# Optimization experiments

Measured on AMD Instinct MI355X. Metric: run time of the kernel, lower is better.

The kernel has to match this reference:

```python
import jax, jax.numpy as jnp
import numpy as np

B, L, T = 32, 512, 400
EMB, PRE, ENC, ARNN, DRNN, NSYM = 512, 256, 512, 1024, 1024, 256
MEAN_COEFF, SCALE_COEFF = 1.0, 10.0


def setup_inputs() -> dict:
    key = jax.random.key(0)
    ks = jax.random.split(key, 20)
    s = 0.02
    inp = {
        'memory': jax.random.normal(ks[0], (B, L, ENC), jnp.float32),
        'decoder_inputs': jax.random.normal(ks[1], (B, EMB, T), jnp.float32),
        'memory_lengths': jax.random.randint(ks[2], (B,), L // 2, L + 1).astype(jnp.int64),
        # prenet
        'pW1': jax.random.normal(ks[3], (PRE, EMB), jnp.float32) * s,
        'pb1': jnp.zeros((PRE,), jnp.float32),
        'pW2': jax.random.normal(ks[4], (PRE, PRE), jnp.float32) * s,
        'pb2': jnp.zeros((PRE,), jnp.float32),
        # attention LSTMCell
        'aWih': jax.random.normal(ks[5], (4 * ARNN, PRE + ENC), jnp.float32) * s,
        'aWhh': jax.random.normal(ks[6], (4 * ARNN, ARNN), jnp.float32) * s,
        'abih': jnp.zeros((4 * ARNN,), jnp.float32),
        'abhh': jnp.zeros((4 * ARNN,), jnp.float32),
        # Gaussian attention param linear (weight zero-init in torch; small here)
        'attWp': jax.random.normal(ks[7], (2, ARNN), jnp.float32) * 0.001,
        'attbp': jnp.zeros((2,), jnp.float32),
        # decoder LSTMCell
        'dWih': jax.random.normal(ks[8], (4 * DRNN, ARNN + ENC), jnp.float32) * s,
        'dWhh': jax.random.normal(ks[9], (4 * DRNN, DRNN), jnp.float32) * s,
        'dbih': jnp.zeros((4 * DRNN,), jnp.float32),
        'dbhh': jnp.zeros((4 * DRNN,), jnp.float32),
        # output linear
        'oW': jax.random.normal(ks[10], (NSYM, DRNN + ENC), jnp.float32) * s,
        'ob': jnp.zeros((NSYM,), jnp.float32),
    }
    return inp


def _lstm_cell(x, h, c, Wih, Whh, bih, bhh):
    g = x @ Wih.T + bih + h @ Whh.T + bhh
    i, f, gg, o = jnp.split(g, 4, axis=-1)
    c = jax.nn.sigmoid(f) * c + jax.nn.sigmoid(i) * jnp.tanh(gg)
    h = jax.nn.sigmoid(o) * jnp.tanh(c)
    return h, c


def _decoder_core(memory, decoder_inputs, memory_lengths,
                  pW1, pb1, pW2, pb2,
                  aWih, aWhh, abih, abhh,
                  attWp, attbp,
                  dWih, dWhh, dbih, dbhh,
                  oW, ob):
    b = memory.shape[0]
    Lm = memory.shape[1]
    # go frame + time-major inputs -> prenet (dropout is identity in eval)
    x = jnp.transpose(decoder_inputs, (2, 0, 1))            # [T, B, EMB]
    x = jnp.concatenate([jnp.zeros((1, b, EMB), x.dtype), x], axis=0)  # [T+1, B, EMB]
    x = jax.nn.relu(x @ pW1.T + pb1)
    x = jax.nn.relu(x @ pW2.T + pb2)                        # [T+1, B, PRE]
    x = x[:T]                                               # loop runs T steps

    lin = jnp.arange(Lm, dtype=memory.dtype)[None, :]       # [1, L]
    pad_mask = lin >= memory_lengths[:, None].astype(memory.dtype)  # [B, L] True at pad

    def step(carry, x_t):
        ah, ac, dh, dc, ctx, mean = carry
        cell_in = jnp.concatenate([x_t, ctx], axis=1)
        ah, ac = _lstm_cell(cell_in, ah, ac, aWih, aWhh, abih, abhh)
        params = ah @ attWp.T + attbp                       # [B, 2]
        mean = mean + jnp.exp(params[:, 0:1]) * MEAN_COEFF  # [B, 1]
        scale = jnp.exp(params[:, 1:2]) * SCALE_COEFF       # [B, 1]
        Z = jnp.sqrt(2.0 * np.pi * scale ** 2)
        w = jnp.exp(-0.5 * (lin - mean) ** 2 / scale ** 2) / Z  # [B, L]
        w = jnp.where(pad_mask, 0.0, w)
        ctx = jnp.einsum('bl,bld->bd', w, memory)           # [B, ENC]
        dec_in = jnp.concatenate([ah, ctx], axis=1)
        dh, dc = _lstm_cell(dec_in, dh, dc, dWih, dWhh, dbih, dbhh)
        out = jnp.concatenate([dh, ctx], axis=1) @ oW.T + ob  # [B, NSYM]
        return (ah, ac, dh, dc, ctx, mean), (out, w, params)

    z = jnp.zeros
    carry0 = (z((b, ARNN)), z((b, ARNN)), z((b, DRNN)), z((b, DRNN)),
              z((b, ENC)), z((b, 1)))
    _, (logits, aligns, ps) = jax.lax.scan(step, carry0, x)
    # time-major -> [B, T, ...]
    return (jnp.transpose(logits, (1, 0, 2)),
            jnp.transpose(aligns, (1, 0, 2)),
            jnp.transpose(ps, (1, 0, 2)))


def reference(memory, decoder_inputs, memory_lengths,
              pW1, pb1, pW2, pb2,
              aWih, aWhh, abih, abhh,
              attWp, attbp,
              dWih, dWhh, dbih, dbhh,
              oW, ob):
    return _decoder_core(memory, decoder_inputs, memory_lengths,
                         pW1, pb1, pW2, pb2,
                         aWih, aWhh, abih, abhh,
                         attWp, attbp,
                         dWih, dWhh, dbih, dbhh,
                         oW, ob)
```

## Files before the change

### kernel.cpp

```cpp
#include <hip/hip_runtime.h>
#include <math.h>

#define Bsz   32
#define Lmem  512
#define Tsteps 400
#define EMBD  512
#define PRE   256
#define ENCD  512
#define ARNN  1024
#define DRNN  1024
#define NSYM  256

typedef _Float16 f16x8 __attribute__((ext_vector_type(8)));
typedef float    f32x4 __attribute__((ext_vector_type(4)));
typedef _Float16 half_t;

#define KA  (PRE + ENCD + ARNN)
#define KAQ (KA / 4)
#define NMA (KAQ / 32)
#define KD  (ARNN + ENCD + DRNN)
#define KDQ (KD / 4)
#define NMD (KDQ / 32)
#define LDA_A 1800
#define LDA_D 2568

__device__ __forceinline__ void st_agent_f16(half_t* p, half_t v) {
    __hip_atomic_store((unsigned short*)p, __builtin_bit_cast(unsigned short, v),
                       __ATOMIC_RELAXED, __HIP_MEMORY_SCOPE_AGENT);
}
__device__ __forceinline__ void st_agent_f32(float* p, float v) {
    __hip_atomic_store(p, v, __ATOMIC_RELAXED, __HIP_MEMORY_SCOPE_AGENT);
}
__device__ __forceinline__ void st_agent_u32(unsigned* p, unsigned v) {
    __hip_atomic_store(p, v, __ATOMIC_RELAXED, __HIP_MEMORY_SCOPE_AGENT);
}
__device__ __forceinline__ float ld_agent_f32(const float* p) {
    return __hip_atomic_load(p, __ATOMIC_RELAXED, __HIP_MEMORY_SCOPE_AGENT);
}
__device__ __forceinline__ unsigned ld_agent_u32(const unsigned* p) {
    return __hip_atomic_load(p, __ATOMIC_RELAXED, __HIP_MEMORY_SCOPE_AGENT);
}
__device__ __forceinline__ f16x8 ld_agent_f16x8(const half_t* p) {
    union { unsigned long long u[2]; f16x8 v; } c;
    c.u[0] = __hip_atomic_load((const unsigned long long*)p,
                               __ATOMIC_RELAXED, __HIP_MEMORY_SCOPE_AGENT);
    c.u[1] = __hip_atomic_load(((const unsigned long long*)p) + 1,
                               __ATOMIC_RELAXED, __HIP_MEMORY_SCOPE_AGENT);
    return c.v;
}

template<int KIH, int KHH>
__global__ __launch_bounds__(256) void conv_lstm_w(
    const float* __restrict__ Wih, const float* __restrict__ Whh,
    const float* __restrict__ bih, const float* __restrict__ bhh,
    half_t* __restrict__ Wcat, float* __restrict__ bsum)
{
    constexpr int K = KIH + KHH;
    const int j = blockIdx.x;
    const float* srcA = Wih + (size_t)j * KIH;
    const float* srcB = Whh + (size_t)j * KHH;
    half_t* dst = Wcat + (size_t)j * K;
    for (int k = threadIdx.x; k < KIH; k += 256) dst[k]       = (half_t)srcA[k];
    for (int k = threadIdx.x; k < KHH; k += 256) dst[KIH + k] = (half_t)srcB[k];
    if (threadIdx.x == 0) bsum[j] = bih[j] + bhh[j];
}

__global__ __launch_bounds__(256) void conv_mat(
    const float* __restrict__ src, half_t* __restrict__ dst, int n)
{
    for (int i = blockIdx.x * 256 + threadIdx.x; i < n; i += gridDim.x * 256)
        dst[i] = (half_t)src[i];
}

__global__ __launch_bounds__(256) void prenet_kernel(
    const float* __restrict__ din,
    const float* __restrict__ pW1, const float* __restrict__ pb1,
    const float* __restrict__ pW2, const float* __restrict__ pb2,
    half_t* __restrict__ xpre)
{
    __shared__ float xs[8][EMBD];
    __shared__ float h1s[8][PRE];
    const int tid = threadIdx.x;
    const int row0 = blockIdx.x * 8;

    for (int idx = tid; idx < 8 * EMBD; idx += 256) {
        int r = idx >> 9;
        int e = idx & 511;
        int rid = row0 + r;
        int t = rid >> 5;
        int b = rid & 31;
        float v = 0.f;
        if (t > 0) v = din[(size_t)b * EMBD * Tsteps + (size_t)e * Tsteps + (t - 1)];
        xs[r][e] = v;
    }
    __syncthreads();

    {
        float acc[8] = {0.f,0.f,0.f,0.f,0.f,0.f,0.f,0.f};
        const float* wr = pW1 + (size_t)tid * EMBD;
        for (int e = 0; e < EMBD; e += 4) {
            float4 wv = *(const float4*)(wr + e);
            #pragma unroll
            for (int r = 0; r < 8; ++r) {
                float4 xv = *(const float4*)&xs[r][e];
                acc[r] += wv.x * xv.x + wv.y * xv.y + wv.z * xv.z + wv.w * xv.w;
            }
        }
        float bias = pb1[tid];
        #pragma unroll
        for (int r = 0; r < 8; ++r) h1s[r][tid] = fmaxf(acc[r] + bias, 0.f);
    }
    __syncthreads();

    {
        float acc[8] = {0.f,0.f,0.f,0.f,0.f,0.f,0.f,0.f};
        const float* wr = pW2 + (size_t)tid * PRE;
        for (int e = 0; e < PRE; e += 4) {
            float4 wv = *(const float4*)(wr + e);
            #pragma unroll
            for (int r = 0; r < 8; ++r) {
                float4 xv = *(const float4*)&h1s[r][e];
                acc[r] += wv.x * xv.x + wv.y * xv.y + wv.z * xv.z + wv.w * xv.w;
            }
        }
        float bias = pb2[tid];
        #pragma unroll
        for (int r = 0; r < 8; ++r) {
            int rid = row0 + r;
            int t = rid >> 5;
            int b = rid & 31;
            xpre[(size_t)t * Bsz * PRE + (size_t)b * PRE + tid] =
                (half_t)fmaxf(acc[r] + bias, 0.f);
        }
    }
}

__device__ __forceinline__ void g_arrive(unsigned* flags, unsigned ph)
{
    asm volatile("s_waitcnt vmcnt(0)" ::: "memory");
    __syncthreads();
    if (threadIdx.x == 0)
        __hip_atomic_store(flags + blockIdx.x * 16, ph,
                           __ATOMIC_RELAXED, __HIP_MEMORY_SCOPE_AGENT);
}
__device__ __forceinline__ void g_wait(unsigned* flags, unsigned ph)
{
    if (threadIdx.x < 64) {
        const unsigned* f = flags + threadIdx.x * 64;
        for (;;) {
            unsigned a = ld_agent_u32(f);
            unsigned b = ld_agent_u32(f + 16);
            unsigned c = ld_agent_u32(f + 32);
            unsigned d = ld_agent_u32(f + 48);
            if (min(min(a, b), min(c, d)) >= ph) break;
            __builtin_amdgcn_s_sleep(2);
        }
    }
    __syncthreads();
}

__global__ __launch_bounds__(512, 1) void decoder_persistent(
    const half_t* __restrict__ Wcat_a, const float* __restrict__ bsum_a,
    const half_t* __restrict__ Wcat_d, const float* __restrict__ bsum_d,
    const half_t* __restrict__ Wo, const float* __restrict__ ob,
    const half_t* __restrict__ xpre,
    const float* __restrict__ attWp, const float* __restrict__ attbp,
    const int* __restrict__ mlen, const half_t* __restrict__ mem16,
    half_t* __restrict__ ah0, half_t* __restrict__ ah1,
    half_t* __restrict__ dh0, half_t* __restrict__ dh1,
    half_t* __restrict__ ctx0, half_t* __restrict__ ctx1,
    float* __restrict__ mean0, float* __restrict__ mean1,
    float* __restrict__ logits, float* __restrict__ aligns,
    float* __restrict__ ps,
    unsigned* flags)
{
    const int blk   = blockIdx.x;
    const int tid   = threadIdx.x;
    const int wave  = tid >> 6;
    const int lane  = tid & 63;
    const int btile = wave & 1;
    const int kq    = wave >> 1;
    const int m15   = lane & 15;
    const int kh    = lane >> 4;
    const int u0    = blk << 2;
    const int bb    = (btile << 4) + m15;

    __shared__ __align__(16) half_t wAl[16 * LDA_A];
    __shared__ __align__(16) half_t wDl[16 * LDA_D];
    __shared__ float gredA[4][2][16][16];
    __shared__ float gredD[4][2][16][16];
    __shared__ float wsh[Lmem];
    __shared__ float lred[16][33];
    __shared__ float wred8[8][2];
    __shared__ float bc2[2];

    for (int g = tid; g < 16 * (KA / 8); g += 512) {
        int r = g / (KA / 8);
        int c = (g - r * (KA / 8)) * 8;
        int jr = (r >> 2) * 1024 + u0 + (r & 3);
        *(f16x8*)(wAl + r * LDA_A + c) = *(const f16x8*)(Wcat_a + (size_t)jr * KA + c);
    }
    for (int g = tid; g < 16 * (KD / 8); g += 512) {
        int r = g / (KD / 8);
        int c = (g - r * (KD / 8)) * 8;
        int jr = (r >> 2) * 1024 + u0 + (r & 3);
        *(f16x8*)(wDl + r * LDA_D + c) = *(const f16x8*)(Wcat_d + (size_t)jr * KD + c);
    }
    float bsA[4] = {0.f,0.f,0.f,0.f}, bsD[4] = {0.f,0.f,0.f,0.f};
    float cA = 0.f, cD = 0.f;
    if (tid < 128) {
        const int ul = tid >> 5;
        #pragma unroll
        for (int gi = 0; gi < 4; ++gi) bsA[gi] = bsum_a[gi * 1024 + u0 + ul];
    } else if (tid < 256) {
        const int ul = (tid - 128) >> 5;
        #pragma unroll
        for (int gi = 0; gi < 4; ++gi) bsD[gi] = bsum_d[gi * 1024 + u0 + ul];
    }
    const half_t* lA = wAl + m15 * LDA_A + kq * KAQ + (kh << 3);
    const half_t* lD = wDl + m15 * LDA_D + kq * KDQ + (kh << 3);
    __syncthreads();

    f16x8 bvA[NMA], bvD[NMD];
    {
        const half_t* s0 = xpre;
        #pragma unroll
        for (int i = 0; i < NMA; ++i) {
            const int kg = kq * KAQ + i * 32 + (kh << 3);
            if (kg < PRE)             bvA[i] = *(const f16x8*)(s0 + bb * PRE + kg);
            else if (kg < PRE + ENCD) bvA[i] = ld_agent_f16x8(ctx1 + bb * ENCD + (kg - PRE));
            else                      bvA[i] = ld_agent_f16x8(ah1 + bb * ARNN + (kg - PRE - ENCD));
        }
    }

    unsigned ph = 0;

    for (int t = 0; t <= Tsteps; ++t) {
        const int par = t & 1;
        half_t*       ah_cur  = par ? ah1 : ah0;
        half_t*       ctx_cur = par ? ctx1 : ctx0;
        const half_t* ctx_prv = par ? ctx0 : ctx1;
        float*        mn_cur  = par ? mean1 : mean0;
        const float*  mn_prv  = par ? mean0 : mean1;
        half_t*       dh_s    = par ? dh0 : dh1;

        if (t < Tsteps) {
            f32x4 accA = {0.f,0.f,0.f,0.f};
            #pragma unroll
            for (int i = 0; i < NMA; ++i) {
                f16x8 av = *(const f16x8*)(lA + i * 32);
                accA = __builtin_amdgcn_mfma_f32_16x16x32_f16(av, bvA[i], accA, 0, 0, 0);
            }
            #pragma unroll
            for (int r = 0; r < 4; ++r)
                gredA[kq][btile][(kh << 2) + r][m15] = accA[r];
        }
        if (t > 0) {
            f32x4 accD = {0.f,0.f,0.f,0.f};
            #pragma unroll
            for (int i = 0; i < NMD; ++i) {
                f16x8 av = *(const f16x8*)(lD + i * 32);
                accD = __builtin_amdgcn_mfma_f32_16x16x32_f16(av, bvD[i], accD, 0, 0, 0);
            }
            #pragma unroll
            for (int r = 0; r < 4; ++r)
                gredD[kq][btile][(kh << 2) + r][m15] = accD[r];
        }
        __syncthreads();
        if (tid < 128) {
            if (t < Tsteps) {
                const int ul = tid >> 5;
                const int bq = tid & 31;
                const int bt = bq >> 4;
                const int nn = bq & 15;
                float g[4];
                #pragma unroll
                for (int gi = 0; gi < 4; ++gi) {
                    const int mr = (gi << 2) + ul;
                    g[gi] = gredA[0][bt][mr][nn] + gredA[1][bt][mr][nn]
                          + gredA[2][bt][mr][nn] + gredA[3][bt][mr][nn] + bsA[gi];
                }
                float si = 1.f / (1.f + expf(-g[0]));
                float sf = 1.f / (1.f + expf(-g[1]));
                float so = 1.f / (1.f + expf(-g[3]));
                cA = sf * cA + si * tanhf(g[2]);
                st_agent_f16(&ah_cur[bq * 1024 + u0 + ul], (half_t)(so * tanhf(cA)));
            }
        } else if (tid < 256) {
            if (t > 0) {
                const int lt = tid - 128;
                const int ul = lt >> 5;
                const int bq = lt & 31;
                const int bt = bq >> 4;
                const int nn = bq & 15;
                float g[4];
                #pragma unroll
                for (int gi = 0; gi < 4; ++gi) {
                    const int mr = (gi << 2) + ul;
                    g[gi] = gredD[0][bt][mr][nn] + gredD[1][bt][mr][nn]
                          + gredD[2][bt][mr][nn] + gredD[3][bt][mr][nn] + bsD[gi];
                }
                float si = 1.f / (1.f + expf(-g[0]));
                float sf = 1.f / (1.f + expf(-g[1]));
                float so = 1.f / (1.f + expf(-g[3]));
                cD = sf * cD + si * tanhf(g[2]);
                st_agent_f16(&dh_s[bq * 1024 + u0 + ul], (half_t)(so * tanhf(cD)));
            }
        }
        ++ph; g_arrive(flags, ph); g_wait(flags, ph);

        if (t < Tsteps) {
            const int abt = blk >> 3;
            const int dt  = blk & 7;
            float p0, p1;
            {
                union { unsigned u; _Float16 h[2]; } a;
                a.u = ld_agent_u32((const unsigned*)(ah_cur + abt * ARNN + 2 * tid));
                float a0 = (float)a.h[0], a1 = (float)a.h[1];
                float2 w0 = *(const float2*)(attWp + 2 * tid);
                float2 w1 = *(const float2*)(attWp + ARNN + 2 * tid);
                p0 = a0 * w0.x + a1 * w0.y;
                p1 = a0 * w1.x + a1 * w1.y;
            }
            #pragma unroll
            for (int off = 32; off > 0; off >>= 1) {
                p0 += __shfl_down(p0, off, 64);
                p1 += __shfl_down(p1, off, 64);
            }
            if (lane == 0) { wred8[wave][0] = p0; wred8[wave][1] = p1; }
            __syncthreads();
            if (tid == 0) {
                float q0 = attbp[0], q1 = attbp[1];
                #pragma unroll
                for (int w = 0; w < 8; ++w) { q0 += wred8[w][0]; q1 += wred8[w][1]; }
                float mn = ld_agent_f32(&mn_prv[abt]) + expf(q0) * 1.0f;
                float sc = expf(q1) * 10.0f;
                if (dt == 0) {
                    st_agent_f32(&mn_cur[abt], mn);
                    st_agent_f32(&ps[(size_t)abt * Tsteps * 2 + (size_t)t * 2 + 0], q0);
                    st_agent_f32(&ps[(size_t)abt * Tsteps * 2 + (size_t)t * 2 + 1], q1);
                }
                bc2[0] = mn; bc2[1] = sc;
            }
            __syncthreads();
            const float mn = bc2[0], sc = bc2[1];
            const float inv_s = 1.f / sc;
            const float coef = 0.3989422804014327f * inv_s;
            const int len = mlen[abt];
            {
                float z = ((float)tid - mn) * inv_s;
                float wv = (tid < len) ? expf(-0.5f * z * z) * coef : 0.f;
                wsh[tid] = wv;
                if (dt == 0)
                    st_agent_f32(&aligns[(size_t)abt * Tsteps * Lmem + (size_t)t * Lmem + tid], wv);
            }
            __syncthreads();
            int lo = (int)fmaxf(0.f, floorf(mn - 9.f * sc));
            int hi = (int)fminf((float)len, ceilf(mn + 9.f * sc) + 1.f);
            const int d8 = (dt << 6) + (wave << 3);
            const half_t* mb = mem16 + (size_t)abt * Lmem * ENCD + d8;
            float acc[8] = {0.f,0.f,0.f,0.f,0.f,0.f,0.f,0.f};
            for (int l = lo + lane; l < hi; l += 64) {
                f16x8 mv = *(const f16x8*)(mb + (size_t)l * ENCD);
                float w = wsh[l];
                #pragma unroll
                for (int j = 0; j < 8; ++j) acc[j] += w * (float)mv[j];
            }
            #pragma unroll
            for (int off = 32; off > 0; off >>= 1) {
                #pragma unroll
                for (int j = 0; j < 8; ++j) acc[j] += __shfl_down(acc[j], off, 64);
            }
            if (lane == 0) {
                #pragma unroll
                for (int j = 0; j < 4; ++j) {
                    union { unsigned u; _Float16 h[2]; } pk;
                    pk.h[0] = (_Float16)acc[2 * j];
                    pk.h[1] = (_Float16)acc[2 * j + 1];
                    st_agent_u32((unsigned*)(ctx_cur + abt * ENCD + d8 + 2 * j), pk.u);
                }
            }
        }
        if (t > 0) {
            const int b_o = tid & 31;
            const int ks  = tid >> 5;
            const half_t* wrow = Wo + (size_t)blk * (DRNN + ENCD) + ks * 96;
            float outacc = 0.f;
            #pragma unroll
            for (int half = 0; half < 2; ++half) {
                f16x8 wv[6], av[6];
                #pragma unroll
                for (int c8 = 0; c8 < 6; ++c8) {
                    const int cc = half * 6 + c8;
                    const int k = ks * 96 + cc * 8;
                    wv[c8] = *(const f16x8*)(wrow + cc * 8);
                    const half_t* ap = (k < DRNN) ? (dh_s + b_o * DRNN + k)
                                                  : (ctx_prv + b_o * ENCD + (k - DRNN));
                    av[c8] = ld_agent_f16x8(ap);
                }
                #pragma unroll
                for (int c8 = 0; c8 < 6; ++c8)
                    #pragma unroll
                    for (int e = 0; e < 8; ++e)
                        outacc += (float)wv[c8][e] * (float)av[c8][e];
            }
            lred[ks][b_o] = outacc;
            __syncthreads();
            if (tid < 32) {
                float s = 0.f;
                #pragma unroll
                for (int q = 0; q < 16; ++q) s += lred[q][tid];
                st_agent_f32(&logits[(size_t)tid * Tsteps * NSYM + (size_t)(t - 1) * NSYM + blk],
                             s + ob[blk]);
            }
        }
        if (t < Tsteps) {
            ++ph; g_arrive(flags, ph);
            if (t + 1 < Tsteps) {
                const half_t* s0n = xpre + (size_t)(t + 1) * Bsz * PRE;
                #pragma unroll
                for (int i = 0; i < NMA; ++i) {
                    const int kg = kq * KAQ + i * 32 + (kh << 3);
                    if (kg < PRE)
                        bvA[i] = *(const f16x8*)(s0n + bb * PRE + kg);
                    else if (kg >= PRE + ENCD)
                        bvA[i] = ld_agent_f16x8(ah_cur + bb * ARNN + (kg - PRE - ENCD));
                }
            }
            #pragma unroll
            for (int i = 0; i < NMD; ++i) {
                const int kg = kq * KDQ + i * 32 + (kh << 3);
                if (kg < ARNN)
                    bvD[i] = ld_agent_f16x8(ah_cur + bb * ARNN + kg);
                else if (kg >= ARNN + ENCD)
                    bvD[i] = ld_agent_f16x8(dh_s + bb * DRNN + (kg - ARNN - ENCD));
            }
            g_wait(flags, ph);
            if (t + 1 < Tsteps) {
                #pragma unroll
                for (int i = 0; i < NMA; ++i) {
                    const int kg = kq * KAQ + i * 32 + (kh << 3);
                    if (kg >= PRE && kg < PRE + ENCD)
                        bvA[i] = ld_agent_f16x8(ctx_cur + bb * ENCD + (kg - PRE));
                }
            }
            #pragma unroll
            for (int i = 0; i < NMD; ++i) {
                const int kg = kq * KDQ + i * 32 + (kh << 3);
                if (kg >= ARNN && kg < ARNN + ENCD)
                    bvD[i] = ld_agent_f16x8(ctx_cur + bb * ENCD + (kg - ARNN));
            }
        }
    }
}

extern "C" void kernel_launch(void* const* d_in, const int* in_sizes, int n_in,
                              void* d_out, int out_size, void* d_ws, size_t ws_size,
                              hipStream_t stream)
{
    (void)in_sizes; (void)n_in; (void)out_size; (void)ws_size;
    const float* memory = (const float*)d_in[0];
    const float* din    = (const float*)d_in[1];
    const int*   mlen   = (const int*)d_in[2];
    const float* pW1    = (const float*)d_in[3];
    const float* pb1    = (const float*)d_in[4];
    const float* pW2    = (const float*)d_in[5];
    const float* pb2    = (const float*)d_in[6];
    const float* aWih   = (const float*)d_in[7];
    const float* aWhh   = (const float*)d_in[8];
    const float* abih   = (const float*)d_in[9];
    const float* abhh   = (const float*)d_in[10];
    const float* attWp  = (const float*)d_in[11];
    const float* attbp  = (const float*)d_in[12];
    const float* dWih   = (const float*)d_in[13];
    const float* dWhh   = (const float*)d_in[14];
    const float* dbih   = (const float*)d_in[15];
    const float* dbhh   = (const float*)d_in[16];
    const float* oW     = (const float*)d_in[17];
    const float* ob     = (const float*)d_in[18];

    float* logits = (float*)d_out;
    float* aligns = logits + (size_t)Bsz * Tsteps * NSYM;
    float* ps     = aligns + (size_t)Bsz * Tsteps * Lmem;

    char* base = (char*)d_ws;
    auto alloc = [&](size_t bytes) -> char* {
        char* p = base; base += (bytes + 255) & ~(size_t)255; return p;
    };
    half_t* Wcat_a = (half_t*)alloc((size_t)4096 * KA * 2);
    half_t* Wcat_d = (half_t*)alloc((size_t)4096 * KD * 2);
    half_t* Wo     = (half_t*)alloc((size_t)NSYM * (DRNN + ENCD) * 2);
    float*  bsum_a = (float*)alloc(4096 * 4);
    float*  bsum_d = (float*)alloc(4096 * 4);
    half_t* xpre   = (half_t*)alloc((size_t)Tsteps * Bsz * PRE * 2);
    half_t* mem16  = (half_t*)alloc((size_t)Bsz * Lmem * ENCD * 2);
    half_t* ah0    = (half_t*)alloc(Bsz * ARNN * 2);
    half_t* ah1    = (half_t*)alloc(Bsz * ARNN * 2);
    half_t* dh0    = (half_t*)alloc(Bsz * DRNN * 2);
    half_t* dh1    = (half_t*)alloc(Bsz * DRNN * 2);
    half_t* ctx0   = (half_t*)alloc(Bsz * ENCD * 2);
    half_t* ctx1   = (half_t*)alloc(Bsz * ENCD * 2);
    float*  mean0  = (float*)alloc(Bsz * 4);
    float*  mean1  = (float*)alloc(Bsz * 4);
    unsigned* flags = (unsigned*)alloc(256 * 16 * 4);

    (void)hipMemsetAsync(ah1,   0, Bsz * ARNN * 2, stream);
    (void)hipMemsetAsync(dh1,   0, Bsz * DRNN * 2, stream);
    (void)hipMemsetAsync(ctx1,  0, Bsz * ENCD * 2, stream);
    (void)hipMemsetAsync(mean0, 0, Bsz * 4, stream);
    (void)hipMemsetAsync(mean1, 0, Bsz * 4, stream);
    (void)hipMemsetAsync(flags, 0, 256 * 16 * 4, stream);

    conv_lstm_w<PRE + ENCD, ARNN><<<4096, 256, 0, stream>>>(
        aWih, aWhh, abih, abhh, Wcat_a, bsum_a);
    conv_lstm_w<ARNN + ENCD, DRNN><<<4096, 256, 0, stream>>>(
        dWih, dWhh, dbih, dbhh, Wcat_d, bsum_d);
    conv_mat<<<768, 256, 0, stream>>>(oW, Wo, NSYM * (DRNN + ENCD));
    conv_mat<<<4096, 256, 0, stream>>>(memory, mem16, Bsz * Lmem * ENCD);
    prenet_kernel<<<Tsteps * Bsz / 8, 256, 0, stream>>>(din, pW1, pb1, pW2, pb2, xpre);

    decoder_persistent<<<256, 512, 0, stream>>>(
        Wcat_a, bsum_a, Wcat_d, bsum_d, Wo, ob, xpre,
        attWp, attbp, mlen, mem16,
        ah0, ah1, dh0, dh1, ctx0, ctx1, mean0, mean1,
        logits, aligns, ps,
        flags);
}
```

Measured before the change: 14.29 ms.

## Replace flat grid barrier with two-level tree barrier and pin prefetched operands

The grid barrier used to have every one of the 256 blocks poll all 256 arrival flags. It is now a hierarchy: 16 aggregator blocks each watch 16 flags, block 0 watches the 16 aggregates, and everyone else polls a single release flag. This cuts polling traffic on the flags in the per-step barrier, but adds two extra serial hops of latency. An empty asm constraint is also added on the prefetched operand vectors so their loads are issued before the barrier and not sunk past it.

```diff
diff --git a/kernel.cpp b/kernel.cpp
--- a/kernel.cpp
+++ b/kernel.cpp
@@ -48,6 +48,7 @@
                                __ATOMIC_RELAXED, __HIP_MEMORY_SCOPE_AGENT);
     return c.v;
 }
+__device__ __forceinline__ void keep16(f16x8& v) { asm volatile("" : "+v"(v)); }
 
 template<int KIH, int KHH>
 __global__ __launch_bounds__(256) void conv_lstm_w(
@@ -140,21 +141,25 @@
     asm volatile("s_waitcnt vmcnt(0)" ::: "memory");
     __syncthreads();
     if (threadIdx.x == 0)
-        __hip_atomic_store(flags + blockIdx.x * 16, ph,
-                           __ATOMIC_RELAXED, __HIP_MEMORY_SCOPE_AGENT);
+        st_agent_u32(flags + blockIdx.x * 16, ph);
 }
 __device__ __forceinline__ void g_wait(unsigned* flags, unsigned ph)
 {
-    if (threadIdx.x < 64) {
-        const unsigned* f = flags + threadIdx.x * 64;
-        for (;;) {
-            unsigned a = ld_agent_u32(f);
-            unsigned b = ld_agent_u32(f + 16);
-            unsigned c = ld_agent_u32(f + 32);
-            unsigned d = ld_agent_u32(f + 48);
-            if (min(min(a, b), min(c, d)) >= ph) break;
-            __builtin_amdgcn_s_sleep(2);
-        }
+    if (blockIdx.x < 16 && threadIdx.x < 16) {
+        const unsigned* f = flags + (blockIdx.x * 16 + threadIdx.x) * 16;
+        while (ld_agent_u32(f) < ph) __builtin_amdgcn_s_sleep(1);
+        if (threadIdx.x == 0)
+            st_agent_u32(flags + (256 + blockIdx.x) * 16, ph);
+    }
+    if (blockIdx.x == 0 && threadIdx.x < 16) {
+        const unsigned* f2 = flags + (256 + threadIdx.x) * 16;
+        while (ld_agent_u32(f2) < ph) __builtin_amdgcn_s_sleep(1);
+        if (threadIdx.x == 0)
+            st_agent_u32(flags + 272 * 16, ph);
+    }
+    if (threadIdx.x == 0) {
+        const unsigned* g = flags + 272 * 16;
+        while (ld_agent_u32(g) < ph) __builtin_amdgcn_s_sleep(1);
     }
     __syncthreads();
 }
@@ -435,6 +440,10 @@
                 else if (kg >= ARNN + ENCD)
                     bvD[i] = ld_agent_f16x8(dh_s + bb * DRNN + (kg - ARNN - ENCD));
             }
+            #pragma unroll
+            for (int i = 0; i < NMA; ++i) keep16(bvA[i]);
+            #pragma unroll
+            for (int i = 0; i < NMD; ++i) keep16(bvD[i]);
             g_wait(flags, ph);
             if (t + 1 < Tsteps) {
                 #pragma unroll
@@ -502,14 +511,14 @@
     half_t* ctx1   = (half_t*)alloc(Bsz * ENCD * 2);
     float*  mean0  = (float*)alloc(Bsz * 4);
     float*  mean1  = (float*)alloc(Bsz * 4);
-    unsigned* flags = (unsigned*)alloc(256 * 16 * 4);
+    unsigned* flags = (unsigned*)alloc(288 * 16 * 4);
 
     (void)hipMemsetAsync(ah1,   0, Bsz * ARNN * 2, stream);
     (void)hipMemsetAsync(dh1,   0, Bsz * DRNN * 2, stream);
     (void)hipMemsetAsync(ctx1,  0, Bsz * ENCD * 2, stream);
     (void)hipMemsetAsync(mean0, 0, Bsz * 4, stream);
     (void)hipMemsetAsync(mean1, 0, Bsz * 4, stream);
-    (void)hipMemsetAsync(flags, 0, 256 * 16 * 4, stream);
+    (void)hipMemsetAsync(flags, 0, 288 * 16 * 4, stream);
 
     conv_lstm_w<PRE + ENCD, ARNN><<<4096, 256, 0, stream>>>(
         aWih, aWhh, abih, abhh, Wcat_a, bsum_a);
```

Result: slower. 15.22 ms (+6.5%).
